# Performance work log

Measured on AMD Instinct MI355X. Metric: run time of the kernel, lower is better.

Reference implementation:

```python
import jax, jax.numpy as jnp
import numpy as np

OUT_H = 7            # roi_layer out_size
OUT_W = 35           # ratio_max(5) * out_size(7); static because rois are built with ceil(max w/h)=5
SAMPLE_NUM = 2       # sampling points per bin edge (sample_num)
STRIDES = (4, 8, 16, 32)


def _rotated_roi_align(feat, rois, spatial_scale, out_h=OUT_H, out_w=OUT_W, ns=SAMPLE_NUM):
    """RoIAlignRotated on one level. rois: [N,6] = [batch_idx, cx, cy, w, h, theta] (image coords)."""
    B, C, H, W = feat.shape
    N = rois.shape[0]
    b = rois[:, 0].astype(jnp.int32)
    cx = rois[:, 1] * spatial_scale
    cy = rois[:, 2] * spatial_scale
    w = jnp.maximum(rois[:, 3] * spatial_scale, 1.0)
    h = jnp.maximum(rois[:, 4] * spatial_scale, 1.0)
    theta = rois[:, 5]
    bin_h = h / out_h
    bin_w = w / out_w
    # sub-bin sample grid (ns x ns samples per output bin), in units of bins
    gy = jnp.arange(out_h, dtype=feat.dtype)[:, None, None, None] + \
        (jnp.arange(ns, dtype=feat.dtype)[None, None, :, None] + 0.5) / ns   # [out_h,1,ns,1]
    gx = jnp.arange(out_w, dtype=feat.dtype)[None, :, None, None] + \
        (jnp.arange(ns, dtype=feat.dtype)[None, None, None, :] + 0.5) / ns   # [1,out_w,1,ns]
    r = lambda v: v[:, None, None, None, None]
    yy = -r(h) * 0.5 + gy[None] * r(bin_h)                 # [N,out_h,1,ns,1]
    xx = -r(w) * 0.5 + gx[None] * r(bin_w)                 # [N,1,out_w,1,ns]
    cos_t, sin_t = r(jnp.cos(theta)), r(jnp.sin(theta))
    x = (xx * cos_t - yy * sin_t + r(cx)).reshape(N, -1)   # [N,P], P = out_h*out_w*ns*ns
    y = (xx * sin_t + yy * cos_t + r(cy)).reshape(N, -1)
    valid = (y >= -1.0) & (y <= H) & (x >= -1.0) & (x <= W)
    y = jnp.clip(y, 0.0, H - 1)
    x = jnp.clip(x, 0.0, W - 1)
    y0 = jnp.floor(y).astype(jnp.int32)
    x0 = jnp.floor(x).astype(jnp.int32)
    y1 = jnp.minimum(y0 + 1, H - 1)
    x1 = jnp.minimum(x0 + 1, W - 1)
    ly = y - y0
    lx = x - x0
    hy = 1.0 - ly
    hx = 1.0 - lx
    bb = b[:, None]
    v = (feat[bb, :, y0, x0] * (hy * hx)[..., None]
         + feat[bb, :, y0, x1] * (hy * lx)[..., None]
         + feat[bb, :, y1, x0] * (ly * hx)[..., None]
         + feat[bb, :, y1, x1] * (ly * lx)[..., None])     # [N,P,C]
    v = v * valid[..., None]
    v = v.reshape(N, out_h, out_w, ns, ns, C).mean(axis=(3, 4))
    return jnp.transpose(v, (0, 3, 1, 2))                  # [N,C,out_h,out_w]


def _forward(feats, rois):
    out = _rotated_roi_align(feats[0], rois, 1.0 / STRIDES[0])
    for f, s in zip(feats[1:], STRIDES[1:]):
        out = jnp.maximum(out, _rotated_roi_align(f, rois, 1.0 / s))
    return out


def setup_inputs() -> dict:
    key = jax.random.key(0)
    ks = jax.random.split(key, 10)
    B, C, N = 2, 256, 512
    feat0 = jax.random.normal(ks[0], (B, C, 256, 256), jnp.float32)
    feat1 = jax.random.normal(ks[1], (B, C, 128, 128), jnp.float32)
    feat2 = jax.random.normal(ks[2], (B, C, 64, 64), jnp.float32)
    feat3 = jax.random.normal(ks[3], (B, C, 32, 32), jnp.float32)
    b = jax.random.randint(ks[4], (N,), 0, B).astype(jnp.float32)
    cx = jax.random.uniform(ks[5], (N,), jnp.float32, 64.0, 960.0)
    cy = jax.random.uniform(ks[6], (N,), jnp.float32, 64.0, 960.0)
    h = jax.random.uniform(ks[7], (N,), jnp.float32, 16.0, 128.0)
    ratio = jax.random.uniform(ks[8], (N,), jnp.float32, 1.01, 4.99)
    ratio = ratio.at[0].set(4.5)  # guarantee ceil(max(w/h)) == 5 -> static out_w = 5*7 = 35
    theta = jax.random.uniform(ks[9], (N,), jnp.float32, 0.0, 1.5)
    rois = jnp.stack([b, cx, cy, h * ratio, h, theta], axis=1)
    return {"feat0": feat0, "feat1": feat1, "feat2": feat2, "feat3": feat3, "rois": rois}


def reference(feat0, feat1, feat2, feat3, rois):
    return _forward((feat0, feat1, feat2, feat3), rois)
```

## Files before the change

### kernel.cpp

```cpp
#include <hip/hip_runtime.h>
#include <hip/hip_bf16.h>
#include <math.h>

#define OUT_H 7
#define OUT_W 35
#define NBINS (OUT_H * OUT_W)
#define NCH   256
#define NROI  512


typedef _Float16 h2_t __attribute__((ext_vector_type(2)));
typedef float    f4_t __attribute__((ext_vector_type(4)));

static __device__ __forceinline__ h2_t as_h2(unsigned u) {
  return __builtin_bit_cast(h2_t, u);
}
static __device__ __forceinline__ unsigned h2_bits(h2_t v) {
  return __builtin_bit_cast(unsigned, v);
}
static __device__ __forceinline__ unsigned pkrtz_bits(float a, float b) {
  return __builtin_bit_cast(unsigned, __builtin_amdgcn_cvt_pkrtz(a, b));
}
static __device__ __forceinline__ unsigned pk_rtn(float a, float b) {
  _Float16 ha = (_Float16)a, hb = (_Float16)b;
  return (unsigned)__builtin_bit_cast(unsigned short, ha) |
         ((unsigned)__builtin_bit_cast(unsigned short, hb) << 16);
}

__global__ __launch_bounds__(256, 8) void transpose_all(
    const float* __restrict__ f0, const float* __restrict__ f1,
    const float* __restrict__ f2, const float* __restrict__ f3,
    ushort* __restrict__ ws)
{
  __shared__ float tile[64 * 65];

  const int t = blockIdx.x;
  int l, rel;
  if      (t < 8192)  { l = 0; rel = t; }
  else if (t < 10240) { l = 1; rel = t - 8192; }
  else if (t < 10752) { l = 2; rel = t - 10240; }
  else                { l = 3; rel = t - 10752; }

  const int HWl  = 65536 >> (2 * l);
  const int lg   = 10 - 2 * l;
  const int hwT  = rel & ((1 << lg) - 1);
  const int rest = rel >> lg;
  const int cT   = rest & 3;
  const int b    = rest >> 2;
  const float* fsrc = (l == 0) ? f0 : (l == 1) ? f1 : (l == 2) ? f2 : f3;
  const int pixoff  = (l == 0) ? 0 : (l == 1) ? 131072 : (l == 2) ? 163840 : 172032;
  const int hw0 = hwT << 6;
  const int c0  = cT << 6;

  const int hwq = threadIdx.x & 15;
  const int r0  = threadIdx.x >> 4;
#pragma unroll
  for (int i = 0; i < 4; ++i) {
    const int r = r0 + 16 * i;
    const f4_t v = __builtin_nontemporal_load(
        (const f4_t*)(fsrc + ((size_t)(b * NCH + c0 + r)) * HWl + hw0 + 4 * hwq));
    float* tp = &tile[r * 65 + 4 * hwq];
    tp[0] = v.x; tp[1] = v.y; tp[2] = v.z; tp[3] = v.w;
  }
  __syncthreads();

  const int cq  = threadIdx.x & 15;
  const int hwl = threadIdx.x >> 4;
  ushort* wp = ws + ((size_t)(pixoff + b * HWl + hw0)) * NCH + c0 + cq * 4;
#pragma unroll
  for (int j = 0; j < 4; ++j) {
    const int hw = hwl + 16 * j;
    const float a0 = tile[(4 * cq + 0) * 65 + hw];
    const float a1 = tile[(4 * cq + 1) * 65 + hw];
    const float a2 = tile[(4 * cq + 2) * 65 + hw];
    const float a3 = tile[(4 * cq + 3) * 65 + hw];
    *(uint2*)(wp + (size_t)hw * NCH) =
        make_uint2(pkrtz_bits(a0, a1), pkrtz_bits(a2, a3));
  }
}

__global__ __launch_bounds__(256, 8) void roi_align_rotated_max(
    const ushort* __restrict__ ft,
    const float* __restrict__ rois,
    float* __restrict__ out)
{
  __shared__ uint4    s_desc[OUT_W * 16];
  __shared__ unsigned s_out[OUT_W * 66];

  const int g    = blockIdx.x;
  const int slot = g & 7;
  const int rest = g >> 3;
  const int hc   = rest % 14;
  const int oh   = hc % 7;
  const int ch2  = hc / 7;
  const int n    = slot + 8 * (rest / 14);

  const float* R = rois + n * 6;
  const int b = (int)R[0];
  const float ct = (float)cos((double)R[5]);
  const float st = (float)sin((double)R[5]);

  for (int j = threadIdx.x; j < OUT_W * 16; j += 256) {
    const int ow = j >> 4;
    const int ls = j & 15;
    const int l  = ls >> 2;
    const int s  = ls & 3;
    const int sy = s >> 1, sx = s & 1;

    const int   Hl     = 256 >> l;
    const float scale  = 0.25f / (float)(1 << l);
    const int   pixoff = (l == 0) ? 0 : (l == 1) ? 131072 : (l == 2) ? 163840 : 172032;

    const float cx = __fmul_rn(R[1], scale);
    const float cy = __fmul_rn(R[2], scale);
    const float w  = fmaxf(__fmul_rn(R[3], scale), 1.0f);
    const float h  = fmaxf(__fmul_rn(R[4], scale), 1.0f);
    const float bin_h = __fdiv_rn(h, (float)OUT_H);
    const float bin_w = __fdiv_rn(w, (float)OUT_W);
    const float gy = (float)oh + (sy ? 0.75f : 0.25f);
    const float gx = (float)ow + (sx ? 0.75f : 0.25f);
    const float yy = __fadd_rn(__fmul_rn(-h, 0.5f), __fmul_rn(gy, bin_h));
    const float xx = __fadd_rn(__fmul_rn(-w, 0.5f), __fmul_rn(gx, bin_w));
    const float x = __fadd_rn(__fsub_rn(__fmul_rn(xx, ct), __fmul_rn(yy, st)), cx);
    const float y = __fadd_rn(__fadd_rn(__fmul_rn(xx, st), __fmul_rn(yy, ct)), cy);

    const bool valid = (y >= -1.0f) && (y <= (float)Hl) &&
                       (x >= -1.0f) && (x <= (float)Hl);
    float yc = fminf(fmaxf(y, 0.0f), (float)(Hl - 1));
    float xc = fminf(fmaxf(x, 0.0f), (float)(Hl - 1));
    int y0 = (int)floorf(yc);
    int x0 = (int)floorf(xc);
    float ly = yc - (float)y0;
    float lx = xc - (float)x0;
    if (y0 >= Hl - 1) { y0 = Hl - 2; ly = 1.0f; }
    if (x0 >= Hl - 1) { x0 = Hl - 2; lx = 1.0f; }
    const float hy = 1.0f - ly, hx = 1.0f - lx;
    const float sc = valid ? 0.25f : 0.0f;

    s_desc[j] = make_uint4(
        (unsigned)((pixoff + (b * Hl + y0) * Hl + x0) * (NCH * 2)),
        pk_rtn(sc * hy * hx, sc * hy * lx),
        pk_rtn(sc * ly * hx, sc * ly * lx), 0u);
  }
  __syncthreads();

  const int wv     = threadIdx.x >> 6;
  const int lane   = threadIdx.x & 63;
  const int volane = ch2 * 256 + lane * 4;

  for (int ow = wv; ow < OUT_W; ow += 4) {
    h2_t m;
#pragma unroll
    for (int l = 0; l < 4; ++l) {
      const int rowb = 131072 >> l;
      h2_t a = {(_Float16)0, (_Float16)0};
#pragma unroll
      for (int s = 0; s < 4; ++s) {
        const uint4 q = s_desc[ow * 16 + l * 4 + s];
        const unsigned off = __builtin_amdgcn_readfirstlane(q.x);
        const char* p0 = (const char*)ft + off;
        const char* p1 = p0 + rowb;
        const unsigned A = *(const unsigned*)(p0 + volane);
        const unsigned B = *(const unsigned*)(p0 + volane + 512);
        const unsigned C = *(const unsigned*)(p1 + volane);
        const unsigned D = *(const unsigned*)(p1 + volane + 512);
        const h2_t w01 = as_h2(q.y), w23 = as_h2(q.z);
        a = __builtin_shufflevector(w01, w01, 0, 0) * as_h2(A) + a;
        a = __builtin_shufflevector(w01, w01, 1, 1) * as_h2(B) + a;
        a = __builtin_shufflevector(w23, w23, 0, 0) * as_h2(C) + a;
        a = __builtin_shufflevector(w23, w23, 1, 1) * as_h2(D) + a;
      }
      if (l == 0) m = a;
      else        m = __builtin_elementwise_max(m, a);
    }
    s_out[ow * 66 + lane] = h2_bits(m);
  }
  __syncthreads();

  const size_t outbase = (size_t)n * NCH * NBINS + (size_t)ch2 * 128 * NBINS +
                         (size_t)oh * OUT_W;
  const _Float16* sh = (const _Float16*)s_out;
#pragma unroll
  for (int j = 0; j < 18; ++j) {
    const int idx = threadIdx.x + j * 256;
    if (idx < 128 * OUT_W) {
      const int cc = idx / OUT_W;
      const int ww = idx - cc * OUT_W;
      out[outbase + (size_t)cc * NBINS + ww] = (float)sh[ww * 132 + cc];
    }
  }
}

extern "C" void kernel_launch(void* const* d_in, const int* in_sizes, int n_in,
                              void* d_out, int out_size, void* d_ws, size_t ws_size,
                              hipStream_t stream) {
  const float* f0 = (const float*)d_in[0];
  const float* f1 = (const float*)d_in[1];
  const float* f2 = (const float*)d_in[2];
  const float* f3 = (const float*)d_in[3];
  const float* rois = (const float*)d_in[4];
  ushort* ws = (ushort*)d_ws;
  float* out = (float*)d_out;

  transpose_all<<<10880, 256, 0, stream>>>(f0, f1, f2, f3, ws);
  roi_align_rotated_max<<<7168, 256, 0, stream>>>(ws, rois, out);
}
```

Before: 464.6 us.

## Split gather lanes across bilinear corners with 8-byte loads and cross-half reduction

The gather loop now has each wave half handle different bilinear corners (x0 vs x1) with 8-byte loads covering four channels per lane. The two halves' partial sums are then combined with a lane-xor-32 shuffle before the per-level max. This widens each memory access and halves the number of load instructions, at the cost of a shuffle and half the lanes idling on the shared-memory store. The ROI kernel is also split into two launches over ROI halves, which adds launch overhead but may improve cache locality.

Result: slower. 477.5 us (+2.8%).

```diff
diff --git a/kernel.cpp b/kernel.cpp
--- a/kernel.cpp
+++ b/kernel.cpp
@@ -25,6 +25,10 @@
   _Float16 ha = (_Float16)a, hb = (_Float16)b;
   return (unsigned)__builtin_bit_cast(unsigned short, ha) |
          ((unsigned)__builtin_bit_cast(unsigned short, hb) << 16);
+}
+static __device__ __forceinline__ h2_t sum32(h2_t v) {
+  const int p = __shfl_xor((int)h2_bits(v), 32, 64);
+  return v + as_h2((unsigned)p);
 }
 
 __global__ __launch_bounds__(256, 8) void transpose_all(
@@ -82,10 +86,11 @@
 __global__ __launch_bounds__(256, 8) void roi_align_rotated_max(
     const ushort* __restrict__ ft,
     const float* __restrict__ rois,
-    float* __restrict__ out)
+    float* __restrict__ out,
+    int n_base)
 {
   __shared__ uint4    s_desc[OUT_W * 16];
-  __shared__ unsigned s_out[OUT_W * 66];
+  __shared__ unsigned s_out[OUT_W * 70];
 
   const int g    = blockIdx.x;
   const int slot = g & 7;
@@ -93,7 +98,7 @@
   const int hc   = rest % 14;
   const int oh   = hc % 7;
   const int ch2  = hc / 7;
-  const int n    = slot + 8 * (rest / 14);
+  const int n    = n_base + slot + 8 * (rest / 14);
 
   const float* R = rois + n * 6;
   const int b = (int)R[0];
@@ -140,40 +145,80 @@
     s_desc[j] = make_uint4(
         (unsigned)((pixoff + (b * Hl + y0) * Hl + x0) * (NCH * 2)),
         pk_rtn(sc * hy * hx, sc * hy * lx),
-        pk_rtn(sc * ly * hx, sc * ly * lx), 0u);
+        pk_rtn(sc * ly * hx, sc * ly * lx),
+        0u);
   }
   __syncthreads();
 
-  const int wv     = threadIdx.x >> 6;
-  const int lane   = threadIdx.x & 63;
-  const int volane = ch2 * 256 + lane * 4;
+  const int wv   = threadIdx.x >> 6;
+  const int lane = threadIdx.x & 63;
+  const char* ftb = (const char*)ft + ch2 * 256 + lane * 8 +
+                    ((lane >= 32) ? 256 : 0);
+  const unsigned wsel = (lane < 32) ? 0x01000100u : 0x03020302u;
 
   for (int ow = wv; ow < OUT_W; ow += 4) {
-    h2_t m;
+    h2_t m0, m1;
 #pragma unroll
     for (int l = 0; l < 4; ++l) {
       const int rowb = 131072 >> l;
-      h2_t a = {(_Float16)0, (_Float16)0};
-#pragma unroll
-      for (int s = 0; s < 4; ++s) {
-        const uint4 q = s_desc[ow * 16 + l * 4 + s];
-        const unsigned off = __builtin_amdgcn_readfirstlane(q.x);
-        const char* p0 = (const char*)ft + off;
-        const char* p1 = p0 + rowb;
-        const unsigned A = *(const unsigned*)(p0 + volane);
-        const unsigned B = *(const unsigned*)(p0 + volane + 512);
-        const unsigned C = *(const unsigned*)(p1 + volane);
-        const unsigned D = *(const unsigned*)(p1 + volane + 512);
-        const h2_t w01 = as_h2(q.y), w23 = as_h2(q.z);
-        a = __builtin_shufflevector(w01, w01, 0, 0) * as_h2(A) + a;
-        a = __builtin_shufflevector(w01, w01, 1, 1) * as_h2(B) + a;
-        a = __builtin_shufflevector(w23, w23, 0, 0) * as_h2(C) + a;
-        a = __builtin_shufflevector(w23, w23, 1, 1) * as_h2(D) + a;
-      }
-      if (l == 0) m = a;
-      else        m = __builtin_elementwise_max(m, a);
+
+      const uint4 q0 = s_desc[ow * 16 + l * 4 + 0];
+      const uint4 q1 = s_desc[ow * 16 + l * 4 + 1];
+      const uint4 q2 = s_desc[ow * 16 + l * 4 + 2];
+      const uint4 q3 = s_desc[ow * 16 + l * 4 + 3];
+
+      uint2 d[8];
+      {
+        const char* p0 = ftb + (int)q0.x;
+        const char* p1 = ftb + (int)q1.x;
+        const char* p2 = ftb + (int)q2.x;
+        const char* p3 = ftb + (int)q3.x;
+        d[0] = *(const uint2*)(p0);
+        d[1] = *(const uint2*)(p0 + rowb);
+        d[2] = *(const uint2*)(p1);
+        d[3] = *(const uint2*)(p1 + rowb);
+        d[4] = *(const uint2*)(p2);
+        d[5] = *(const uint2*)(p2 + rowb);
+        d[6] = *(const uint2*)(p3);
+        d[7] = *(const uint2*)(p3 + rowb);
+      }
+
+      h2_t a0 = {(_Float16)0, (_Float16)0};
+      h2_t a1 = {(_Float16)0, (_Float16)0};
+      {
+        const h2_t wy0 = as_h2(__builtin_amdgcn_perm(q0.y, q0.y, wsel));
+        const h2_t wy1 = as_h2(__builtin_amdgcn_perm(q0.z, q0.z, wsel));
+        a0 = wy0 * as_h2(d[0].x) + a0;  a1 = wy0 * as_h2(d[0].y) + a1;
+        a0 = wy1 * as_h2(d[1].x) + a0;  a1 = wy1 * as_h2(d[1].y) + a1;
+      }
+      {
+        const h2_t wy0 = as_h2(__builtin_amdgcn_perm(q1.y, q1.y, wsel));
+        const h2_t wy1 = as_h2(__builtin_amdgcn_perm(q1.z, q1.z, wsel));
+        a0 = wy0 * as_h2(d[2].x) + a0;  a1 = wy0 * as_h2(d[2].y) + a1;
+        a0 = wy1 * as_h2(d[3].x) + a0;  a1 = wy1 * as_h2(d[3].y) + a1;
+      }
+      {
+        const h2_t wy0 = as_h2(__builtin_amdgcn_perm(q2.y, q2.y, wsel));
+        const h2_t wy1 = as_h2(__builtin_amdgcn_perm(q2.z, q2.z, wsel));
+        a0 = wy0 * as_h2(d[4].x) + a0;  a1 = wy0 * as_h2(d[4].y) + a1;
+        a0 = wy1 * as_h2(d[5].x) + a0;  a1 = wy1 * as_h2(d[5].y) + a1;
+      }
+      {
+        const h2_t wy0 = as_h2(__builtin_amdgcn_perm(q3.y, q3.y, wsel));
+        const h2_t wy1 = as_h2(__builtin_amdgcn_perm(q3.z, q3.z, wsel));
+        a0 = wy0 * as_h2(d[6].x) + a0;  a1 = wy0 * as_h2(d[6].y) + a1;
+        a0 = wy1 * as_h2(d[7].x) + a0;  a1 = wy1 * as_h2(d[7].y) + a1;
+      }
+
+      const h2_t r0 = sum32(a0), r1 = sum32(a1);
+      if (l == 0) { m0 = r0; m1 = r1; }
+      else {
+        m0 = __builtin_elementwise_max(m0, r0);
+        m1 = __builtin_elementwise_max(m1, r1);
+      }
     }
-    s_out[ow * 66 + lane] = h2_bits(m);
+    if (lane < 32)
+      *(uint2*)&s_out[ow * 70 + lane * 2] = make_uint2(h2_bits(m0), h2_bits(m1));
   }
   __syncthreads();
 
@@ -186,7 +231,7 @@
     if (idx < 128 * OUT_W) {
       const int cc = idx / OUT_W;
       const int ww = idx - cc * OUT_W;
-      out[outbase + (size_t)cc * NBINS + ww] = (float)sh[ww * 132 + cc];
+      out[outbase + (size_t)cc * NBINS + ww] = (float)sh[ww * 140 + cc];
     }
   }
 }
@@ -203,5 +248,6 @@
   float* out = (float*)d_out;
 
   transpose_all<<<10880, 256, 0, stream>>>(f0, f1, f2, f3, ws);
-  roi_align_rotated_max<<<7168, 256, 0, stream>>>(ws, rois, out);
-}
+  roi_align_rotated_max<<<3584, 256, 0, stream>>>(ws, rois, out, 0);
+  roi_align_rotated_max<<<3584, 256, 0, stream>>>(ws, rois, out, 256);
+}
```
